# Performance work log

Hardware: AMD Instinct MI355X
Metric: run time of the kernel (lower is better)

## Reference

```python
import jax, jax.numpy as jnp
import numpy as np

# PDE constants (from init_kwargs)
D_C = 1.0      # diffusion coefficient D
K_C = 1.0      # xi * z * e
V_C = 0.1      # v_const (convection)
NS = 3         # len(sdim), sdim = [0,1,2] (contiguous spatial dims)
TDIM = 3       # time dimension index


def _net(y, W0, b0, W1, b1, W2, b2, W3, b3, Wo, bo):
    # per-sample MLP: y (4,) -> (2,) = (c, Fi)
    h = jnp.tanh(y @ W0 + b0)
    h = jnp.tanh(h @ W1 + b1)
    h = jnp.tanh(h @ W2 + b2)
    h = jnp.tanh(h @ W3 + b3)
    return h @ Wo + bo


def setup_inputs() -> dict:
    key = jax.random.key(0)
    ks = jax.random.split(key, 8)
    B, DIN, H, DOUT = 16384, 4, 256, 2

    def w(k, shape):
        return (jax.random.normal(k, shape, jnp.float32)
                * np.float32(1.0 / np.sqrt(shape[0])))

    return {
        "x": jax.random.normal(ks[0], (B, DIN), jnp.float32),
        "W0": w(ks[1], (DIN, H)), "b0": jnp.zeros((H,), jnp.float32),
        "W1": w(ks[2], (H, H)),   "b1": jnp.zeros((H,), jnp.float32),
        "W2": w(ks[3], (H, H)),   "b2": jnp.zeros((H,), jnp.float32),
        "W3": w(ks[4], (H, H)),   "b3": jnp.zeros((H,), jnp.float32),
        "Wo": w(ks[5], (H, DOUT)), "bo": jnp.zeros((DOUT,), jnp.float32),
    }


def reference(x, W0, b0, W1, b1, W2, b2, W3, b3, Wo, bo):
    def single(xi):
        f = lambda y: _net(y, W0, b0, W1, b1, W2, b2, W3, b3, Wo, bo)
        out = f(xi)                          # (2,)  = (c, Fi)
        jac = jax.jacrev(f)(xi)              # (2, 4): batch_jacobian[...,0,:]
        Hm = jax.jacfwd(jax.jacrev(f))(xi)   # (2, 4, 4): per-output Hessian

        c, Fi = out[0], out[1]
        c_jac, Fi_jac = jac[0], jac[1]
        c_t = c_jac[TDIM]                    # time derivative
        c_grd = c_jac[:NS]                   # spatial gradient of c
        Fi_grd = Fi_jac[:NS]                 # spatial gradient of Fi
        Hc_s = Hm[0, :NS, :NS]               # spatial Hessian of c
        HFi_s = Hm[1, :NS, :NS]              # spatial Hessian of Fi

        Fi_lap = jnp.trace(HFi_s)            # Laplacian of Fi
        # j = -D*c_grd - K*c*Fi_grd + c*v_const ; div over spatial dims:
        # d j_i/d x_i = -D Hc[i,i] - K (c_grd_i Fi_grd_i + c HFi[i,i]) + v c_grd_i
        j_div = (-D_C * jnp.trace(Hc_s)
                 - K_C * (jnp.dot(c_grd, Fi_grd) + c * Fi_lap)
                 + V_C * jnp.sum(c_grd))
        return c, c_t, c_grd, Fi, Fi_grd, Fi_lap, j_div

    c, c_t, c_grd, Fi, Fi_grd, Fi_lap, j_div = jax.vmap(single)(x)
    return (c[:, None], c_t, c_grd, Fi[:, None], Fi_grd,
            Fi_lap[:, None], j_div[:, None])
```

## Files before the change

kernel.cpp:

```cpp
#include <hip/hip_runtime.h>

#define HDIM  256
#define YP    264
#define SPBM  8
#define MROWS (SPBM * 8)

typedef unsigned short u16;
typedef __attribute__((ext_vector_type(8))) short  short8;
typedef __attribute__((ext_vector_type(4))) float  f32x4;



__device__ __forceinline__ float bf2f(u16 u) {
    union { unsigned int i; float f; } v; v.i = ((unsigned int)u) << 16; return v.f;
}
__device__ __forceinline__ u16 f2bf(float f) {
    union { float f; unsigned int u; } v; v.f = f;
    return (u16)((v.u + 0x8000u) >> 16);
}
__device__ __forceinline__ u16 f2bf_rne(float f) {
    union { float f; unsigned int u; } v; v.f = f;
    unsigned int r = v.u + 0x7fffu + ((v.u >> 16) & 1u);
    return (u16)(r >> 16);
}
__device__ __forceinline__ float fast_tanh(float x) {
    const float e = __builtin_amdgcn_exp2f(x * 2.885390081777927f);
    const float r = __builtin_amdgcn_rcpf(e + 1.f);
    return 1.f - 2.f * r;
}

__global__ __launch_bounds__(256)
void prep_w(const float* __restrict__ W1, const float* __restrict__ W2,
            const float* __restrict__ W3, const float* __restrict__ Wo,
            u16* __restrict__ ws) {
    const int bid = blockIdx.x;
    const int tid = threadIdx.x;
    if (bid == 96) {
#pragma unroll
        for (int oc = 0; oc < 2; ++oc)
            ws[3 * 65536 + oc * 256 + tid] = f2bf_rne(Wo[tid * 2 + oc]);
        return;
    }
    const int which = bid >> 5;
    const int tile  = bid & 31;
    const int k0 = (tile & 7) * 32;
    const int n0 = (tile >> 3) * 64;
    const float* W = (which == 0) ? W1 : ((which == 1) ? W2 : W3);
    __shared__ float T[32][65];
    const int rk = tid >> 4;
    const int rn = (tid & 15) * 4;
#pragma unroll
    for (int rep = 0; rep < 2; ++rep) {
        const float4 v = *(const float4*)(W + (k0 + rep * 16 + rk) * 256 + n0 + rn);
        T[rep * 16 + rk][rn + 0] = v.x;
        T[rep * 16 + rk][rn + 1] = v.y;
        T[rep * 16 + rk][rn + 2] = v.z;
        T[rep * 16 + rk][rn + 3] = v.w;
    }
    __syncthreads();
    const int tl = tid >> 6;
    const int ln = tid & 63;
    const int nn = tl * 16 + (ln & 15);
    const int kb = ((ln >> 4) & 3) * 8;
    short8 o;
#pragma unroll
    for (int j = 0; j < 8; ++j)
        o[j] = (short)f2bf_rne(T[kb + j][nn]);
    const int t_glob = (n0 >> 4) + tl;
    *(short8*)(ws + which * 65536 + ((t_glob * 8 + (tile & 7)) * 64 + ln) * 8) = o;
}

__device__ __forceinline__ void hidden_layer_mfma(u16* __restrict__ Y,
                                                  const u16* __restrict__ Wt,
                                                  const float* __restrict__ b,
                                                  int l, int wv) {
    const int lm    = l & 15;
    const int lk8   = (l >> 4) * 8;
    const int nbase = wv * 64;
    const u16* bsrc = Wt + (wv * 4) * 4096 + l * 8;

    f32x4 acc[4][4];
#pragma unroll
    for (int mt = 0; mt < 4; ++mt)
#pragma unroll
        for (int nt = 0; nt < 4; ++nt) acc[mt][nt] = (f32x4){0.f, 0.f, 0.f, 0.f};

#pragma unroll
    for (int ks = 0; ks < 8; ++ks) {
        const int kk = ks * 32 + lk8;
        short8 a[4], bf[4];
#pragma unroll
        for (int mt = 0; mt < 4; ++mt)
            a[mt] = *(const short8*)(Y + (mt * 16 + lm) * YP + kk);
#pragma unroll
        for (int nt = 0; nt < 4; ++nt)
            bf[nt] = *(const short8*)(bsrc + nt * 4096 + ks * 512);
#pragma unroll
        for (int mt = 0; mt < 4; ++mt)
#pragma unroll
            for (int nt = 0; nt < 4; ++nt)
                acc[mt][nt] = __builtin_amdgcn_mfma_f32_16x16x32_bf16(
                    a[mt], bf[nt], acc[mt][nt], 0, 0, 0);
    }

    float bias[4];
#pragma unroll
    for (int nt = 0; nt < 4; ++nt) bias[nt] = b[nbase + nt * 16 + lm];

    __syncthreads();

    const int g = l >> 4;
#pragma unroll
    for (int half = 0; half < 2; ++half) {
#pragma unroll
        for (int nt = 0; nt < 4; ++nt) {
            const f32x4 ulo = acc[2 * half + 0][nt];
            const f32x4 uhi = acc[2 * half + 1][nt];
            const float ty = fast_tanh(ulo[0] + bias[nt]);
            const float t  = 1.f - ty * ty;
            const float m  = -2.f * ty * t;
            const int n = nbase + nt * 16 + lm;
            u16* ylo = Y + (half * 32 + 4 * g) * YP + n;
            u16* yhi = ylo + 16 * YP;
            ylo[0 * YP] = f2bf(ty);
            ylo[1 * YP] = f2bf(t * ulo[1]);
            ylo[2 * YP] = f2bf(t * ulo[2]);
            ylo[3 * YP] = f2bf(t * ulo[3]);
            yhi[0 * YP] = f2bf(t * uhi[0]);
            yhi[1 * YP] = f2bf(t * uhi[1] + m * ulo[1] * ulo[1]);
            yhi[2 * YP] = f2bf(t * uhi[2] + m * ulo[2] * ulo[2]);
            yhi[3 * YP] = f2bf(t * uhi[3] + m * ulo[3] * ulo[3]);
        }
    }
    __syncthreads();
}

__global__ __launch_bounds__(256, 4)
void mlp_jet_mfma(const float* __restrict__ x,
                  const float* __restrict__ W0, const float* __restrict__ b0,
                  const float* __restrict__ b1, const float* __restrict__ b2,
                  const float* __restrict__ b3, const float* __restrict__ bo,
                  const u16* __restrict__ Wt,
                  float* __restrict__ out, int nB) {
    __shared__ __align__(16) u16 Y[MROWS * YP];
    __shared__ float4 xs4[SPBM];
    __shared__ float  part[MROWS][2];

    const int tid = threadIdx.x;
    const int wv  = tid >> 6;
    const int l   = tid & 63;
    const int lm  = l & 15;
    const int lk8 = (l >> 4) * 8;
    const int n0  = blockIdx.x * SPBM;

    if (tid < SPBM) xs4[tid] = *(const float4*)(x + (n0 + tid) * 4);
    __syncthreads();
    {
        const int n = tid;
        const float w0 = W0[0 * HDIM + n], w1 = W0[1 * HDIM + n];
        const float w2 = W0[2 * HDIM + n], w3 = W0[3 * HDIM + n];
        const float bb = b0[n];
#pragma unroll
        for (int s = 0; s < SPBM; ++s) {
            const float4 xv = xs4[s];
            const float u  = xv.x * w0 + xv.y * w1 + xv.z * w2 + xv.w * w3 + bb;
            const float ty = fast_tanh(u);
            const float t  = 1.f - ty * ty;
            const float m  = -2.f * ty * t;
            u16* ylo = Y + (32 * (s >> 2) + 4 * (s & 3)) * YP + n;
            u16* yhi = ylo + 16 * YP;
            ylo[0 * YP] = f2bf(ty);
            ylo[1 * YP] = f2bf(t * w0);
            ylo[2 * YP] = f2bf(t * w1);
            ylo[3 * YP] = f2bf(t * w2);
            yhi[0 * YP] = f2bf(t * w3);
            yhi[1 * YP] = f2bf(m * w0 * w0);
            yhi[2 * YP] = f2bf(m * w1 * w1);
            yhi[3 * YP] = f2bf(m * w2 * w2);
        }
    }
    __syncthreads();

    hidden_layer_mfma(Y, Wt + 0 * 65536, b1, l, wv);
    hidden_layer_mfma(Y, Wt + 1 * 65536, b2, l, wv);
    hidden_layer_mfma(Y, Wt + 2 * 65536, b3, l, wv);

    {
        const u16* wob = Wt + 3 * 65536;
        f32x4 h = (f32x4){0.f, 0.f, 0.f, 0.f};
#pragma unroll
        for (int ks = 0; ks < 8; ++ks) {
            const int kk = ks * 32 + lk8;
            const short8 a = *(const short8*)(Y + (wv * 16 + lm) * YP + kk);
            short8 bfr = (short8){0,0,0,0,0,0,0,0};
            if (lm < 2) bfr = *(const short8*)(wob + lm * 256 + kk);
            h = __builtin_amdgcn_mfma_f32_16x16x32_bf16(a, bfr, h, 0, 0, 0);
        }
        if (lm < 2) {
#pragma unroll
            for (int r = 0; r < 4; ++r)
                part[wv * 16 + (l >> 4) * 4 + r][lm] = h[r];
        }
    }
    __syncthreads();

    if (tid < SPBM) {
        const int s = tid;
        float q0[8], q1[8];
#pragma unroll
        for (int ch = 0; ch < 8; ++ch) {
            const int R = 32 * (s >> 2) + 16 * (ch >> 2) + 4 * (s & 3) + (ch & 3);
            q0[ch] = part[R][0];
            q1[ch] = part[R][1];
        }
        const float c0  = q0[0] + bo[0];
        const float Fi  = q1[0] + bo[1];
        const float cg0 = q0[1], cg1 = q0[2], cg2 = q0[3];
        const float ct  = q0[4];
        const float fg0 = q1[1], fg1 = q1[2], fg2 = q1[3];
        const float trHc  = q0[5] + q0[6] + q0[7];
        const float fiLap = q1[5] + q1[6] + q1[7];
        const float jd = -trHc
                         - (cg0 * fg0 + cg1 * fg1 + cg2 * fg2 + c0 * fiLap)
                         + 0.1f * (cg0 + cg1 + cg2);
        const int n = n0 + s;
        out[0 * nB + n]         = c0;
        out[1 * nB + n]         = ct;
        out[2 * nB + 3 * n + 0] = cg0;
        out[2 * nB + 3 * n + 1] = cg1;
        out[2 * nB + 3 * n + 2] = cg2;
        out[5 * nB + n]         = Fi;
        out[6 * nB + 3 * n + 0] = fg0;
        out[6 * nB + 3 * n + 1] = fg1;
        out[6 * nB + 3 * n + 2] = fg2;
        out[9 * nB + n]         = fiLap;
        out[10 * nB + n]        = jd;
    }
}

extern "C" void kernel_launch(void* const* d_in, const int* in_sizes, int n_in,
                              void* d_out, int out_size, void* d_ws, size_t ws_size,
                              hipStream_t stream) {
    const float* x  = (const float*)d_in[0];
    const float* W0 = (const float*)d_in[1];
    const float* b0 = (const float*)d_in[2];
    const float* W1 = (const float*)d_in[3];
    const float* b1 = (const float*)d_in[4];
    const float* W2 = (const float*)d_in[5];
    const float* b2 = (const float*)d_in[6];
    const float* W3 = (const float*)d_in[7];
    const float* b3 = (const float*)d_in[8];
    const float* Wo = (const float*)d_in[9];
    const float* bo = (const float*)d_in[10];
    float* out = (float*)d_out;
    u16*   Wt  = (u16*)d_ws;

    const int nB = in_sizes[0] / 4;

    hipLaunchKernelGGL(prep_w, dim3(97), dim3(256), 0, stream, W1, W2, W3, Wo, Wt);
    hipLaunchKernelGGL(mlp_jet_mfma, dim3(nB / SPBM), dim3(256), 0, stream,
                       x, W0, b0, b1, b2, b3, bo, Wt, out, nB);
}
```

Before: 127.3 us.

## Permute weight columns so epilogue writes packed 8-byte bf16 vectors via cvt_pk

```diff
diff --git a/kernel.cpp b/kernel.cpp
--- a/kernel.cpp
+++ b/kernel.cpp
@@ -10,18 +10,15 @@
 typedef __attribute__((ext_vector_type(4))) float  f32x4;
 
 
-
-__device__ __forceinline__ float bf2f(u16 u) {
-    union { unsigned int i; float f; } v; v.i = ((unsigned int)u) << 16; return v.f;
-}
-__device__ __forceinline__ u16 f2bf(float f) {
-    union { float f; unsigned int u; } v; v.f = f;
-    return (u16)((v.u + 0x8000u) >> 16);
-}
 __device__ __forceinline__ u16 f2bf_rne(float f) {
     union { float f; unsigned int u; } v; v.f = f;
     unsigned int r = v.u + 0x7fffu + ((v.u >> 16) & 1u);
     return (u16)(r >> 16);
+}
+__device__ __forceinline__ unsigned int cvtpk(float a, float b) {
+    unsigned int r;
+    asm("v_cvt_pk_bf16_f32 %0, %1, %2" : "=v"(r) : "v"(a), "v"(b));
+    return r;
 }
 __device__ __forceinline__ float fast_tanh(float x) {
     const float e = __builtin_amdgcn_exp2f(x * 2.885390081777927f);
@@ -60,7 +57,7 @@
     __syncthreads();
     const int tl = tid >> 6;
     const int ln = tid & 63;
-    const int nn = tl * 16 + (ln & 15);
+    const int nn = 4 * (ln & 15) + tl;
     const int kb = ((ln >> 4) & 3) * 8;
     short8 o;
 #pragma unroll
@@ -103,33 +100,40 @@
                     a[mt], bf[nt], acc[mt][nt], 0, 0, 0);
     }
 
-    float bias[4];
-#pragma unroll
-    for (int nt = 0; nt < 4; ++nt) bias[nt] = b[nbase + nt * 16 + lm];
+    const float4 b4 = *(const float4*)(b + nbase + 4 * lm);
 
     __syncthreads();
 
     const int g = l >> 4;
 #pragma unroll
     for (int half = 0; half < 2; ++half) {
-#pragma unroll
-        for (int nt = 0; nt < 4; ++nt) {
-            const f32x4 ulo = acc[2 * half + 0][nt];
-            const f32x4 uhi = acc[2 * half + 1][nt];
-            const float ty = fast_tanh(ulo[0] + bias[nt]);
-            const float t  = 1.f - ty * ty;
-            const float m  = -2.f * ty * t;
-            const int n = nbase + nt * 16 + lm;
-            u16* ylo = Y + (half * 32 + 4 * g) * YP + n;
-            u16* yhi = ylo + 16 * YP;
-            ylo[0 * YP] = f2bf(ty);
-            ylo[1 * YP] = f2bf(t * ulo[1]);
-            ylo[2 * YP] = f2bf(t * ulo[2]);
-            ylo[3 * YP] = f2bf(t * ulo[3]);
-            yhi[0 * YP] = f2bf(t * uhi[0]);
-            yhi[1 * YP] = f2bf(t * uhi[1] + m * ulo[1] * ulo[1]);
-            yhi[2 * YP] = f2bf(t * uhi[2] + m * ulo[2] * ulo[2]);
-            yhi[3 * YP] = f2bf(t * uhi[3] + m * ulo[3] * ulo[3]);
+        unsigned int pk[2][8];
+#pragma unroll
+        for (int pr = 0; pr < 2; ++pr) {
+            const int na = 2 * pr, nb = 2 * pr + 1;
+            const float bba = (pr == 0) ? b4.x : b4.z;
+            const float bbb = (pr == 0) ? b4.y : b4.w;
+            const float ty0 = fast_tanh(acc[2 * half][na][0] + bba);
+            const float ty1 = fast_tanh(acc[2 * half][nb][0] + bbb);
+            const float t0 = 1.f - ty0 * ty0, t1 = 1.f - ty1 * ty1;
+            const float m0 = -2.f * ty0 * t0, m1 = -2.f * ty1 * t1;
+            pk[pr][0] = cvtpk(ty0, ty1);
+            pk[pr][4] = cvtpk(t0 * acc[2 * half + 1][na][0],
+                              t1 * acc[2 * half + 1][nb][0]);
+#pragma unroll
+            for (int j = 1; j < 4; ++j) {
+                const float a0 = acc[2 * half][na][j];
+                const float a1 = acc[2 * half][nb][j];
+                pk[pr][j]     = cvtpk(t0 * a0, t1 * a1);
+                pk[pr][4 + j] = cvtpk(t0 * acc[2 * half + 1][na][j] + m0 * a0 * a0,
+                                      t1 * acc[2 * half + 1][nb][j] + m1 * a1 * a1);
+            }
+        }
+        u16* yrow = Y + (half * 32 + 4 * g) * YP + nbase + 4 * lm;
+#pragma unroll
+        for (int j = 0; j < 4; ++j) {
+            *(uint2*)(yrow + j * YP)        = (uint2){pk[0][j],     pk[1][j]};
+            *(uint2*)(yrow + (16 + j) * YP) = (uint2){pk[0][4 + j], pk[1][4 + j]};
         }
     }
     __syncthreads();
@@ -155,28 +159,40 @@
 
     if (tid < SPBM) xs4[tid] = *(const float4*)(x + (n0 + tid) * 4);
     __syncthreads();
-    {
-        const int n = tid;
-        const float w0 = W0[0 * HDIM + n], w1 = W0[1 * HDIM + n];
-        const float w2 = W0[2 * HDIM + n], w3 = W0[3 * HDIM + n];
-        const float bb = b0[n];
-#pragma unroll
-        for (int s = 0; s < SPBM; ++s) {
-            const float4 xv = xs4[s];
-            const float u  = xv.x * w0 + xv.y * w1 + xv.z * w2 + xv.w * w3 + bb;
-            const float ty = fast_tanh(u);
-            const float t  = 1.f - ty * ty;
-            const float m  = -2.f * ty * t;
-            u16* ylo = Y + (32 * (s >> 2) + 4 * (s & 3)) * YP + n;
-            u16* yhi = ylo + 16 * YP;
-            ylo[0 * YP] = f2bf(ty);
-            ylo[1 * YP] = f2bf(t * w0);
-            ylo[2 * YP] = f2bf(t * w1);
-            ylo[3 * YP] = f2bf(t * w2);
-            yhi[0 * YP] = f2bf(t * w3);
-            yhi[1 * YP] = f2bf(m * w0 * w0);
-            yhi[2 * YP] = f2bf(m * w1 * w1);
-            yhi[3 * YP] = f2bf(m * w2 * w2);
+#pragma unroll
+    for (int rep = 0; rep < 2; ++rep) {
+        const int idx = tid + 256 * rep;
+        const int s   = idx >> 6;
+        const int cg  = idx & 63;
+        const float4 xv = xs4[s];
+        unsigned int pk[2][8];
+#pragma unroll
+        for (int pr = 0; pr < 2; ++pr) {
+            const int c = 4 * cg + 2 * pr;
+            const float2 w0 = *(const float2*)(W0 + 0 * HDIM + c);
+            const float2 w1 = *(const float2*)(W0 + 1 * HDIM + c);
+            const float2 w2 = *(const float2*)(W0 + 2 * HDIM + c);
+            const float2 w3 = *(const float2*)(W0 + 3 * HDIM + c);
+            const float2 bb = *(const float2*)(b0 + c);
+            const float u0 = xv.x*w0.x + xv.y*w1.x + xv.z*w2.x + xv.w*w3.x + bb.x;
+            const float u1 = xv.x*w0.y + xv.y*w1.y + xv.z*w2.y + xv.w*w3.y + bb.y;
+            const float ty0 = fast_tanh(u0), ty1 = fast_tanh(u1);
+            const float t0 = 1.f - ty0 * ty0, t1 = 1.f - ty1 * ty1;
+            const float m0 = -2.f * ty0 * t0, m1 = -2.f * ty1 * t1;
+            pk[pr][0] = cvtpk(ty0, ty1);
+            pk[pr][1] = cvtpk(t0 * w0.x, t1 * w0.y);
+            pk[pr][2] = cvtpk(t0 * w1.x, t1 * w1.y);
+            pk[pr][3] = cvtpk(t0 * w2.x, t1 * w2.y);
+            pk[pr][4] = cvtpk(t0 * w3.x, t1 * w3.y);
+            pk[pr][5] = cvtpk(m0 * w0.x * w0.x, m1 * w0.y * w0.y);
+            pk[pr][6] = cvtpk(m0 * w1.x * w1.x, m1 * w1.y * w1.y);
+            pk[pr][7] = cvtpk(m0 * w2.x * w2.x, m1 * w2.y * w2.y);
+        }
+        u16* yr = Y + (32 * (s >> 2) + 4 * (s & 3)) * YP + 4 * cg;
+#pragma unroll
+        for (int j = 0; j < 4; ++j) {
+            *(uint2*)(yr + j * YP)        = (uint2){pk[0][j],     pk[1][j]};
+            *(uint2*)(yr + (16 + j) * YP) = (uint2){pk[0][4 + j], pk[1][4 + j]};
         }
     }
     __syncthreads();
```

Result: no change. 125.6 us (median of 2 runs) (-1.3%).
